# Performance work log

Hardware: AMD Instinct MI355X
Metric: run time of the kernel (lower is better)

Reference implementation:

```python
import jax, jax.numpy as jnp
import numpy as np

P, N, B, F, H, O, D, A = 3, 6144, 3072, 512, 8, 32, 256, 128
HI = F // H  # per-head input dim = 64


def setup_inputs() -> dict:
    key = jax.random.key(0)
    ks = jax.random.split(key, 12)
    s = 0.05
    return dict(
        features=jax.random.normal(ks[0], (P, N, F), jnp.float32),
        biases=jax.random.normal(ks[1], (P, N, N), jnp.float32),
        batch_nodes=jax.random.randint(ks[2], (P, B), 0, N),
        RL_thresholds=jax.random.uniform(ks[3], (P, 1), jnp.float32),
        Wc1=jax.random.normal(ks[4], (P, H, O, HI), jnp.float32) * s,
        bc1=jnp.zeros((P, H, O), jnp.float32),
        a1=jax.random.normal(ks[5], (P, H, O), jnp.float32) * s,
        ab1=jnp.zeros((P, H), jnp.float32),
        a2=jax.random.normal(ks[6], (P, H, O), jnp.float32) * s,
        ab2=jnp.zeros((P, H), jnp.float32),
        Wm=jax.random.normal(ks[7], (D, D), jnp.float32) * s,
        bm=jnp.zeros((D,), jnp.float32),
        w_omega=jax.random.normal(ks[8], (D, A), jnp.float32) * s,
        b_omega=jnp.zeros((A,), jnp.float32),
        u_omega=jax.random.normal(ks[9], (A,), jnp.float32) * s,
    )


def reference(features, biases, batch_nodes, RL_thresholds, Wc1, bc1, a1, ab1,
              a2, ab2, Wm, bm, w_omega, b_omega, u_omega):
    embeds = []
    for i in range(P):  # fixed small relation loop (bias_mx_len)
        idx = batch_nodes[i]
        bf = features[i][idx]                      # [B, F]
        bb = biases[i][idx][:, idx]                # [B, B] bias mask
        xh = bf.reshape(B, H, HI).transpose(1, 0, 2)   # [H, B, HI] per-head feature slices
        # Attn_Head: conv1d(k=1) == per-head linear projection
        seq = jnp.einsum('hbi,hoi->hbo', xh, Wc1[i]) + bc1[i][:, None, :]  # [H, B, O]
        f1 = jnp.einsum('hbo,ho->hb', seq, a1[i]) + ab1[i][:, None]       # [H, B]
        f2 = jnp.einsum('hbo,ho->hb', seq, a2[i]) + ab2[i][:, None]       # [H, B]
        logits = jax.nn.leaky_relu(f1[:, :, None] + f2[:, None, :], 0.01)  # [H, B, B]
        coefs = jax.nn.softmax(logits + bb[None], axis=-1)                 # [H, B, B]
        out = jax.nn.elu(jnp.einsum('hqk,hko->hqo', coefs, seq))           # [H, B, O]
        h1 = out.transpose(1, 0, 2).reshape(B, H * O)                      # concat heads -> [B, D]
        embeds.append(h1 @ Wm.T + bm)                                      # w_multi
    multi = jnp.stack(embeds, axis=1)              # [B, P, D]
    inputs = multi * RL_thresholds[None]           # RL scaling, [P,1] broadcasts
    # SimpleAttnLayer: semantic attention over relations
    v = jnp.tanh(jnp.einsum('bpd,da->bpa', inputs, w_omega) + b_omega)
    vu = jnp.einsum('bpa,a->bp', v, u_omega)
    alphas = jax.nn.softmax(vu, axis=-1)           # [B, P]
    return jnp.sum(inputs * alphas[:, :, None], axis=1)  # [B, D]
```

## Files before the change

### kernel.cpp

```cpp
#include <hip/hip_runtime.h>
#include <cstdint>
#include <cstddef>

#define PP 3
#define NN 6144
#define BB 3072
#define FF 512
#define HH 8
#define OO 32
#define DD 256
#define AA 128
#define M0 10.0f
#define KSPLIT 4
#define KRANGE (BB/KSPLIT)
#define NT (KRANGE/32)

typedef __attribute__((ext_vector_type(8))) short short8;
typedef __attribute__((ext_vector_type(4))) float f32x4;

__device__ __forceinline__ unsigned short f2bf(float x){
  union { float f; unsigned u; } v; v.f = x;
  unsigned r = v.u + 0x7fffu + ((v.u >> 16) & 1u);
  return (unsigned short)(r >> 16);
}

__device__ __forceinline__ f32x4 mfma16(short8 a, short8 b, f32x4 c){
  return __builtin_amdgcn_mfma_f32_16x16x32_bf16(a, b, c, 0, 0, 0);
}

__global__ __launch_bounds__(256) void k_seq(
    const float* __restrict__ features, const int* __restrict__ batch_nodes,
    const float* __restrict__ Wc1, const float* __restrict__ bc1,
    const float* __restrict__ a1, const float* __restrict__ ab1,
    const float* __restrict__ a2, const float* __restrict__ ab2,
    unsigned short* __restrict__ seqT, float* __restrict__ f1g, float* __restrict__ f2T)
{
  int i = blockIdx.z, h = blockIdx.y, b0 = blockIdx.x * 8;
  int t = threadIdx.x;
  __shared__ float xs[8][64];
  __shared__ float wt[64][33];
  __shared__ float a1s[32], a2s[32], bcs[32];
  __shared__ float sst[32][9];
  const float* W = Wc1 + (size_t)(i*HH + h) * OO * 64;
  for (int e = t; e < 2048; e += 256){ int o = e >> 6, c = e & 63; wt[c][o] = W[e]; }
  if (t < 32){
    a1s[t] = a1[(i*HH+h)*OO + t];
    a2s[t] = a2[(i*HH+h)*OO + t];
    bcs[t] = bc1[(i*HH+h)*OO + t];
  }
  for (int e = t; e < 512; e += 256){
    int bl = e >> 6, c = e & 63;
    int row = batch_nodes[i*BB + b0 + bl];
    xs[bl][c] = features[((size_t)i*NN + row)*FF + h*64 + c];
  }
  __syncthreads();
  int bl = t >> 5, o = t & 31;
  float acc = bcs[o];
  #pragma unroll
  for (int c = 0; c < 64; c++) acc += xs[bl][c] * wt[c][o];
  float v1 = acc * a1s[o], v2 = acc * a2s[o];
  #pragma unroll
  for (int s = 16; s >= 1; s >>= 1){ v1 += __shfl_xor(v1, s); v2 += __shfl_xor(v2, s); }
  if (o == 0){
    f1g[(i*HH+h)*BB + b0 + bl] = v1 + ab1[i*HH+h];
    f2T[((size_t)i*BB + b0 + bl)*HH + h] = v2 + ab2[i*HH+h];
  }
  sst[o][bl] = acc;
  __syncthreads();
  {
    int o2 = t >> 3, b2 = t & 7;
    seqT[((size_t)(i*HH+h)*OO + o2)*BB + b0 + b2] = f2bf(sst[o2][b2]);
  }
}

__global__ __launch_bounds__(256) void k_gather(
    const float* __restrict__ biases, const int* __restrict__ batch_nodes,
    const float* __restrict__ f1g, const float* __restrict__ f2T,
    float* __restrict__ bbg, float* __restrict__ linv, int i_base, int nbuf)
{
  int i = i_base + blockIdx.z;
  int q0 = blockIdx.x * 2;
  int t = threadIdx.x;
  __shared__ float rowbuf[2][NN];
  __shared__ float wred[4][2][HH];
  int r0 = batch_nodes[i*BB + q0];
  int r1 = batch_nodes[i*BB + q0 + 1];
  const float4* s0 = (const float4*)(biases + ((size_t)i*NN + r0)*NN);
  const float4* s1 = (const float4*)(biases + ((size_t)i*NN + r1)*NN);
  #pragma unroll
  for (int e = 0; e < NN/4; e += 256){
    ((float4*)rowbuf[0])[e + t] = s0[e + t];
    ((float4*)rowbuf[1])[e + t] = s1[e + t];
  }
  float f1h[2][HH], lh[2][HH];
  #pragma unroll
  for (int h = 0; h < HH; h++){
    f1h[0][h] = f1g[(i*HH+h)*BB + q0];
    f1h[1][h] = f1g[(i*HH+h)*BB + q0 + 1];
    lh[0][h] = 0.f; lh[1][h] = 0.f;
  }
  const int* ci = batch_nodes + i*BB;
  float* dst0 = bbg + ((size_t)(i % nbuf)*BB + q0)*BB;
  float* dst1 = dst0 + BB;
  __syncthreads();
  for (int c = 0; c < BB; c += 256){
    int k = c + t;
    int col = ci[k];
    float b0v = rowbuf[0][col];
    float b1v = rowbuf[1][col];
    dst0[k] = b0v; dst1[k] = b1v;
    const float4* fp = (const float4*)(f2T + ((size_t)i*BB + k)*HH);
    float4 fa = fp[0], fb = fp[1];
    float f2v[8] = {fa.x,fa.y,fa.z,fa.w,fb.x,fb.y,fb.z,fb.w};
    #pragma unroll
    for (int h = 0; h < HH; h++){
      float s0v = f1h[0][h] + f2v[h]; s0v = (s0v >= 0.f ? s0v : 0.01f*s0v) + b0v;
      float s1v = f1h[1][h] + f2v[h]; s1v = (s1v >= 0.f ? s1v : 0.01f*s1v) + b1v;
      lh[0][h] += __expf(s0v - M0);
      lh[1][h] += __expf(s1v - M0);
    }
  }
  #pragma unroll
  for (int r = 0; r < 2; r++)
  #pragma unroll
  for (int h = 0; h < HH; h++){
    float v = lh[r][h];
    #pragma unroll
    for (int s = 32; s >= 1; s >>= 1) v += __shfl_xor(v, s);
    if ((t & 63) == 0) wred[t >> 6][r][h] = v;
  }
  __syncthreads();
  if (t < 16){
    int r = t >> 3, h = t & 7;
    float L = wred[0][r][h] + wred[1][r][h] + wred[2][r][h] + wred[3][r][h];
    linv[(i*HH+h)*BB + q0 + r] = 1.f / L;
  }
}

__global__ __launch_bounds__(256, 4) void k_attn(
    const float* __restrict__ bbg, const unsigned short* __restrict__ seqT,
    const float* __restrict__ f1g, const float* __restrict__ f2T,
    const float* __restrict__ linv, float* __restrict__ h1p, int i_base, int nbuf)
{
  int i = i_base + blockIdx.z;
  int ks = blockIdx.y;
  int q0 = blockIdx.x * 32;
  int kbase = ks * KRANGE;
  int t = threadIdx.x;
  int w = t >> 6, lane = t & 63;
  int qf = lane & 15, kq = lane >> 4;
  __shared__ float bbt[2][32][33];
  __shared__ float f2t[2][32][9];
  f32x4 acc[2][2][2] = {};
  float f1r[2][2], lir[2][2];
  #pragma unroll
  for (int hh = 0; hh < 2; hh++)
  #pragma unroll
  for (int qh = 0; qh < 2; qh++){
    int h = w*2 + hh;
    f1r[hh][qh] = f1g[(i*HH+h)*BB + q0 + qh*16 + qf];
    lir[hh][qh] = linv[(i*HH+h)*BB + q0 + qh*16 + qf];
  }
  const float* bbb = bbg + (size_t)(i % nbuf)*BB*BB;

  auto ld = [&](int k0, float rb[4], float &rf, short8 rs[4]){
    #pragma unroll
    for (int j = 0; j < 4; j++){ int e = j*256 + t; int r = e >> 5, c = e & 31;
      rb[j] = bbb[(size_t)(q0 + r)*BB + k0 + c]; }
    { int c = t >> 3, h = t & 7; rf = f2T[((size_t)i*BB + k0 + c)*HH + h]; }
    #pragma unroll
    for (int hh = 0; hh < 2; hh++){
      const unsigned short* sp = seqT + ((size_t)(i*HH + w*2 + hh)*OO)*BB + k0 + kq*8;
      rs[hh*2+0] = *(const short8*)(sp + (size_t)qf*BB);
      rs[hh*2+1] = *(const short8*)(sp + (size_t)(qf+16)*BB);
    }
  };
  auto st = [&](int buf, float rb[4], float rf){
    #pragma unroll
    for (int j = 0; j < 4; j++){ int e = j*256 + t; int r = e >> 5, c = e & 31; bbt[buf][r][c] = rb[j]; }
    { int c = t >> 3, h = t & 7; f2t[buf][c][h] = rf; }
  };
  auto comp = [&](int buf, short8 rs[4]){
    #pragma unroll
    for (int hh = 0; hh < 2; hh++){
      int h = w*2 + hh;
      int kk = kq*8;
      short8 af0, af1;
      #pragma unroll
      for (int j = 0; j < 8; j++){
        float f2v = f2t[buf][kk+j][h];
        float s0 = f1r[hh][0] + f2v; s0 = (s0 >= 0.f ? s0 : 0.01f*s0) + bbt[buf][qf][kk+j];
        float s1 = f1r[hh][1] + f2v; s1 = (s1 >= 0.f ? s1 : 0.01f*s1) + bbt[buf][qf+16][kk+j];
        af0[j] = (short)f2bf(__expf(s0 - M0) * lir[hh][0]);
        af1[j] = (short)f2bf(__expf(s1 - M0) * lir[hh][1]);
      }
      acc[hh][0][0] = mfma16(af0, rs[hh*2+0], acc[hh][0][0]);
      acc[hh][0][1] = mfma16(af0, rs[hh*2+1], acc[hh][0][1]);
      acc[hh][1][0] = mfma16(af1, rs[hh*2+0], acc[hh][1][0]);
      acc[hh][1][1] = mfma16(af1, rs[hh*2+1], acc[hh][1][1]);
    }
  };

  float rbbA[4], rf2A; short8 rsqA[4];
  float rbbB[4], rf2B; short8 rsqB[4];
  ld(kbase, rbbA, rf2A, rsqA);
  st(0, rbbA, rf2A);
  __syncthreads();
  for (int it = 0; it < NT; it += 2){
    int k1 = kbase + (it+1)*32;
    int k2 = (it+2 < NT) ? kbase + (it+2)*32 : kbase;
    ld(k1, rbbB, rf2B, rsqB);
    comp(0, rsqA);
    st(1, rbbB, rf2B);
    __syncthreads();
    ld(k2, rbbA, rf2A, rsqA);
    comp(1, rsqB);
    st(0, rbbA, rf2A);
    __syncthreads();
  }
  #pragma unroll
  for (int hh = 0; hh < 2; hh++){
    int h = w*2 + hh;
    #pragma unroll
    for (int qh = 0; qh < 2; qh++)
    #pragma unroll
    for (int oh = 0; oh < 2; oh++)
    #pragma unroll
    for (int r = 0; r < 4; r++){
      int q = q0 + qh*16 + kq*4 + r;
      int o = qf + oh*16;
      h1p[(((size_t)ks*PP + i)*BB + q)*DD + h*OO + o] = acc[hh][qh][oh][r];
    }
  }
}

__global__ __launch_bounds__(256) void k_twm(const float* __restrict__ Wm, float* __restrict__ wmT){
  int e = blockIdx.x, d = threadIdx.x;
  wmT[(size_t)e*DD + d] = Wm[(size_t)d*DD + e];
}

__global__ __launch_bounds__(256) void k_final(
    const float* __restrict__ h1p, const float* __restrict__ wmT, const float* __restrict__ bm,
    const float* __restrict__ RL, const float* __restrict__ w_omega, const float* __restrict__ b_omega,
    const float* __restrict__ u_omega, float* __restrict__ out)
{
  __shared__ float buf[48*256];
  __shared__ float wred[4][24];
  __shared__ float alph[3][16];
  const size_t PB = (size_t)PP*BB*DD;
  int t = threadIdx.x;
  int lane = t & 63, w = t >> 6;
  int b0 = blockIdx.x * 16;
  for (int e = t; e < 48*256; e += 256){
    int pb = e >> 8, d = e & 255;
    int p = pb / 16, bl = pb & 15;
    size_t off = ((size_t)p*BB + b0 + bl)*DD + d;
    float v = h1p[off] + h1p[off + PB] + h1p[off + 2*PB] + h1p[off + 3*PB];
    buf[e] = (v > 0.f) ? v : (__expf(v) - 1.f);
  }
  __syncthreads();
  float acc[48];
  #pragma unroll
  for (int x = 0; x < 48; x++) acc[x] = 0.f;
  for (int e = 0; e < 256; e += 4){
    float w0 = wmT[(e+0)*DD + t];
    float w1 = wmT[(e+1)*DD + t];
    float w2 = wmT[(e+2)*DD + t];
    float w3 = wmT[(e+3)*DD + t];
    #pragma unroll
    for (int pb = 0; pb < 48; pb++){
      float4 hv = *(const float4*)&buf[pb*256 + e];
      acc[pb] += hv.x*w0 + hv.y*w1 + hv.z*w2 + hv.w*w3;
    }
  }
  __syncthreads();
  {
    float bmv = bm[t];
    #pragma unroll
    for (int p = 0; p < 3; p++){
      float rl = RL[p];
      #pragma unroll
      for (int bl = 0; bl < 16; bl++)
        buf[(p*16+bl)*256 + t] = (acc[p*16+bl] + bmv) * rl;
    }
  }
  __syncthreads();
  int a = t & 127, g = t >> 7;
  float acc2[24];
  #pragma unroll
  for (int x = 0; x < 24; x++) acc2[x] = 0.f;
  for (int e = 0; e < 256; e += 4){
    float w0 = w_omega[(e+0)*AA + a];
    float w1 = w_omega[(e+1)*AA + a];
    float w2 = w_omega[(e+2)*AA + a];
    float w3 = w_omega[(e+3)*AA + a];
    #pragma unroll
    for (int p = 0; p < 3; p++){
      #pragma unroll
      for (int bl = 0; bl < 8; bl++){
        float4 iv = *(const float4*)&buf[(p*16 + g*8 + bl)*256 + e];
        acc2[p*8+bl] += iv.x*w0 + iv.y*w1 + iv.z*w2 + iv.w*w3;
      }
    }
  }
  {
    float bo = b_omega[a], uo = u_omega[a];
    #pragma unroll
    for (int x = 0; x < 24; x++){
      float v = tanhf(acc2[x] + bo) * uo;
      #pragma unroll
      for (int s = 32; s >= 1; s >>= 1) v += __shfl_xor(v, s);
      if (lane == 0) wred[w][x] = v;
    }
  }
  __syncthreads();
  if (t < 16){
    int b = t;
    int g2 = b >> 3, bl2 = b & 7;
    float vu[3];
    #pragma unroll
    for (int p = 0; p < 3; p++){
      int j = p*8 + bl2;
      vu[p] = wred[g2*2 + 0][j] + wred[g2*2 + 1][j];
    }
    float mx = fmaxf(vu[0], fmaxf(vu[1], vu[2]));
    float e0 = __expf(vu[0]-mx), e1 = __expf(vu[1]-mx), e2 = __expf(vu[2]-mx);
    float inv = 1.f / (e0+e1+e2);
    alph[0][b] = e0*inv; alph[1][b] = e1*inv; alph[2][b] = e2*inv;
  }
  __syncthreads();
  #pragma unroll
  for (int bl = 0; bl < 16; bl++){
    float o = buf[(0*16+bl)*256 + t]*alph[0][bl]
            + buf[(1*16+bl)*256 + t]*alph[1][bl]
            + buf[(2*16+bl)*256 + t]*alph[2][bl];
    out[(size_t)(b0+bl)*DD + t] = o;
  }
}

extern "C" void kernel_launch(void* const* d_in, const int* in_sizes, int n_in,
                              void* d_out, int out_size, void* d_ws, size_t ws_size,
                              hipStream_t stream)
{
  const float* features = (const float*)d_in[0];
  const float* biases   = (const float*)d_in[1];
  const int*   batch_nodes = (const int*)d_in[2];
  const float* RL   = (const float*)d_in[3];
  const float* Wc1  = (const float*)d_in[4];
  const float* bc1  = (const float*)d_in[5];
  const float* a1   = (const float*)d_in[6];
  const float* ab1  = (const float*)d_in[7];
  const float* a2   = (const float*)d_in[8];
  const float* ab2  = (const float*)d_in[9];
  const float* Wm   = (const float*)d_in[10];
  const float* bm   = (const float*)d_in[11];
  const float* w_omega = (const float*)d_in[12];
  const float* b_omega = (const float*)d_in[13];
  const float* u_omega = (const float*)d_in[14];
  float* out = (float*)d_out;

  size_t sz_bbg1 = (size_t)BB*BB*4;
  size_t sz_seqT = (size_t)PP*HH*OO*BB*2;
  size_t sz_f    = (size_t)PP*HH*BB*4;
  size_t sz_h1   = (size_t)PP*BB*DD*4;
  size_t sz_wmT  = (size_t)DD*DD*4;
  size_t fixed = sz_seqT + 3*sz_f + (size_t)KSPLIT*sz_h1 + sz_wmT + 16*256;
  int nbuf = (ws_size >= fixed + 3*sz_bbg1 + 256) ? 3 : 1;

  char* p = (char*)d_ws;
  auto take = [&](size_t bytes)->char*{ char* r = p; p += (bytes + 255) & ~(size_t)255; return r; };
  float* bbg  = (float*)take(sz_bbg1 * (size_t)nbuf);
  unsigned short* seqT = (unsigned short*)take(sz_seqT);
  float* f1g  = (float*)take(sz_f);
  float* f2T  = (float*)take(sz_f);
  float* linv = (float*)take(sz_f);
  float* h1p  = (float*)take(sz_h1 * (size_t)KSPLIT);
  float* wmT  = (float*)take(sz_wmT);

  k_twm<<<dim3(DD), dim3(DD), 0, stream>>>(Wm, wmT);
  k_seq<<<dim3(BB/8, HH, PP), dim3(256), 0, stream>>>(features, batch_nodes, Wc1, bc1, a1, ab1, a2, ab2, seqT, f1g, f2T);
  int nloop = (nbuf == 3) ? 1 : 3;
  int z = (nbuf == 3) ? 3 : 1;
  for (int r = 0; r < nloop; r++){
    k_gather<<<dim3(BB/2, 1, z), dim3(256), 0, stream>>>(biases, batch_nodes, f1g, f2T, bbg, linv, r, nbuf);
    k_attn<<<dim3(BB/32, KSPLIT, z), dim3(256), 0, stream>>>(bbg, seqT, f1g, f2T, linv, h1p, r, nbuf);
  }
  k_final<<<dim3(BB/16), dim3(256), 0, stream>>>(h1p, wmT, bm, RL, w_omega, b_omega, u_omega, out);
}
```

Before: 928.1 us.

## Defer softmax normalization: accumulate row sums in attention kernel, normalize in final

Removes the per-row exp-sum pass from the gather kernel, which now only copies and pre-shifts the bias by M0. The attention kernel accumulates unnormalized exp sums alongside the MFMA products, writes per-split partial sums, and the final kernel divides the combined output by the summed denominators before ELU. This cuts a full pass of exp work over B×B×H elements and the f2T reads in gather. The cost is extra adds in the attention inner loop and a small extra buffer. Precision changes slightly because unnormalized values are rounded to bf16 before the MFMA, and the bf16 conversion now uses the library intrinsic instead of the hand-written rounding.

After: 1.093 ms. +17.8%, slower.

```diff
diff --git a/kernel.cpp b/kernel.cpp
--- a/kernel.cpp
+++ b/kernel.cpp
@@ -1,4 +1,5 @@
 #include <hip/hip_runtime.h>
+#include <hip/hip_bf16.h>
 #include <cstdint>
 #include <cstddef>
 
@@ -24,6 +25,10 @@
   return (unsigned short)(r >> 16);
 }
 
+__device__ __forceinline__ short f2bf_n(float x){
+  return __builtin_bit_cast(short, __float2bfloat16(x));
+}
+
 __device__ __forceinline__ f32x4 mfma16(short8 a, short8 b, f32x4 c){
   return __builtin_amdgcn_mfma_f32_16x16x32_bf16(a, b, c, 0, 0, 0);
 }
@@ -75,14 +80,12 @@
 
 __global__ __launch_bounds__(256) void k_gather(
     const float* __restrict__ biases, const int* __restrict__ batch_nodes,
-    const float* __restrict__ f1g, const float* __restrict__ f2T,
-    float* __restrict__ bbg, float* __restrict__ linv, int i_base, int nbuf)
+    float* __restrict__ bbg, int i_base, int nbuf)
 {
   int i = i_base + blockIdx.z;
   int q0 = blockIdx.x * 2;
   int t = threadIdx.x;
   __shared__ float rowbuf[2][NN];
-  __shared__ float wred[4][2][HH];
   int r0 = batch_nodes[i*BB + q0];
   int r1 = batch_nodes[i*BB + q0 + 1];
   const float4* s0 = (const float4*)(biases + ((size_t)i*NN + r0)*NN);
@@ -92,55 +95,23 @@
     ((float4*)rowbuf[0])[e + t] = s0[e + t];
     ((float4*)rowbuf[1])[e + t] = s1[e + t];
   }
-  float f1h[2][HH], lh[2][HH];
-  #pragma unroll
-  for (int h = 0; h < HH; h++){
-    f1h[0][h] = f1g[(i*HH+h)*BB + q0];
-    f1h[1][h] = f1g[(i*HH+h)*BB + q0 + 1];
-    lh[0][h] = 0.f; lh[1][h] = 0.f;
-  }
   const int* ci = batch_nodes + i*BB;
   float* dst0 = bbg + ((size_t)(i % nbuf)*BB + q0)*BB;
   float* dst1 = dst0 + BB;
   __syncthreads();
+  #pragma unroll 4
   for (int c = 0; c < BB; c += 256){
     int k = c + t;
     int col = ci[k];
-    float b0v = rowbuf[0][col];
-    float b1v = rowbuf[1][col];
-    dst0[k] = b0v; dst1[k] = b1v;
-    const float4* fp = (const float4*)(f2T + ((size_t)i*BB + k)*HH);
-    float4 fa = fp[0], fb = fp[1];
-    float f2v[8] = {fa.x,fa.y,fa.z,fa.w,fb.x,fb.y,fb.z,fb.w};
-    #pragma unroll
-    for (int h = 0; h < HH; h++){
-      float s0v = f1h[0][h] + f2v[h]; s0v = (s0v >= 0.f ? s0v : 0.01f*s0v) + b0v;
-      float s1v = f1h[1][h] + f2v[h]; s1v = (s1v >= 0.f ? s1v : 0.01f*s1v) + b1v;
-      lh[0][h] += __expf(s0v - M0);
-      lh[1][h] += __expf(s1v - M0);
-    }
-  }
-  #pragma unroll
-  for (int r = 0; r < 2; r++)
-  #pragma unroll
-  for (int h = 0; h < HH; h++){
-    float v = lh[r][h];
-    #pragma unroll
-    for (int s = 32; s >= 1; s >>= 1) v += __shfl_xor(v, s);
-    if ((t & 63) == 0) wred[t >> 6][r][h] = v;
-  }
-  __syncthreads();
-  if (t < 16){
-    int r = t >> 3, h = t & 7;
-    float L = wred[0][r][h] + wred[1][r][h] + wred[2][r][h] + wred[3][r][h];
-    linv[(i*HH+h)*BB + q0 + r] = 1.f / L;
+    dst0[k] = rowbuf[0][col] - M0;
+    dst1[k] = rowbuf[1][col] - M0;
   }
 }
 
 __global__ __launch_bounds__(256, 4) void k_attn(
     const float* __restrict__ bbg, const unsigned short* __restrict__ seqT,
     const float* __restrict__ f1g, const float* __restrict__ f2T,
-    const float* __restrict__ linv, float* __restrict__ h1p, int i_base, int nbuf)
+    float* __restrict__ Lp, float* __restrict__ h1p, int i_base, int nbuf)
 {
   int i = i_base + blockIdx.z;
   int ks = blockIdx.y;
@@ -152,14 +123,14 @@
   __shared__ float bbt[2][32][33];
   __shared__ float f2t[2][32][9];
   f32x4 acc[2][2][2] = {};
-  float f1r[2][2], lir[2][2];
+  float Ls[2][2] = {{0.f,0.f},{0.f,0.f}};
+  float f1r[2][2];
   #pragma unroll
   for (int hh = 0; hh < 2; hh++)
   #pragma unroll
   for (int qh = 0; qh < 2; qh++){
     int h = w*2 + hh;
     f1r[hh][qh] = f1g[(i*HH+h)*BB + q0 + qh*16 + qf];
-    lir[hh][qh] = linv[(i*HH+h)*BB + q0 + qh*16 + qf];
   }
   const float* bbb = bbg + (size_t)(i % nbuf)*BB*BB;
 
@@ -191,8 +162,10 @@
         float f2v = f2t[buf][kk+j][h];
         float s0 = f1r[hh][0] + f2v; s0 = (s0 >= 0.f ? s0 : 0.01f*s0) + bbt[buf][qf][kk+j];
         float s1 = f1r[hh][1] + f2v; s1 = (s1 >= 0.f ? s1 : 0.01f*s1) + bbt[buf][qf+16][kk+j];
-        af0[j] = (short)f2bf(__expf(s0 - M0) * lir[hh][0]);
-        af1[j] = (short)f2bf(__expf(s1 - M0) * lir[hh][1]);
+        float e0 = __expf(s0), e1 = __expf(s1);
+        Ls[hh][0] += e0; Ls[hh][1] += e1;
+        af0[j] = f2bf_n(e0);
+        af1[j] = f2bf_n(e1);
       }
       acc[hh][0][0] = mfma16(af0, rs[hh*2+0], acc[hh][0][0]);
       acc[hh][0][1] = mfma16(af0, rs[hh*2+1], acc[hh][0][1]);
@@ -219,6 +192,16 @@
     __syncthreads();
   }
   #pragma unroll
+  for (int hh = 0; hh < 2; hh++)
+  #pragma unroll
+  for (int qh = 0; qh < 2; qh++){
+    float v = Ls[hh][qh];
+    v += __shfl_xor(v, 16);
+    v += __shfl_xor(v, 32);
+    if (kq == 0)
+      Lp[(((size_t)ks*PP + i)*HH + w*2 + hh)*BB + q0 + qh*16 + qf] = v;
+  }
+  #pragma unroll
   for (int hh = 0; hh < 2; hh++){
     int h = w*2 + hh;
     #pragma unroll
@@ -240,22 +223,34 @@
 }
 
 __global__ __launch_bounds__(256) void k_final(
-    const float* __restrict__ h1p, const float* __restrict__ wmT, const float* __restrict__ bm,
+    const float* __restrict__ h1p, const float* __restrict__ Lp,
+    const float* __restrict__ wmT, const float* __restrict__ bm,
     const float* __restrict__ RL, const float* __restrict__ w_omega, const float* __restrict__ b_omega,
     const float* __restrict__ u_omega, float* __restrict__ out)
 {
   __shared__ float buf[48*256];
   __shared__ float wred[4][24];
   __shared__ float alph[3][16];
+  __shared__ float linvs[48][8];
   const size_t PB = (size_t)PP*BB*DD;
+  const size_t KL = (size_t)PP*HH*BB;
   int t = threadIdx.x;
   int lane = t & 63, w = t >> 6;
   int b0 = blockIdx.x * 16;
+  for (int e = t; e < 48*8; e += 256){
+    int pb = e >> 3, h = e & 7;
+    int p = pb / 16, bl = pb & 15;
+    size_t off = ((size_t)p*HH + h)*BB + b0 + bl;
+    float L = Lp[off] + Lp[off+KL] + Lp[off+2*KL] + Lp[off+3*KL];
+    linvs[pb][h] = 1.f / L;
+  }
+  __syncthreads();
   for (int e = t; e < 48*256; e += 256){
     int pb = e >> 8, d = e & 255;
     int p = pb / 16, bl = pb & 15;
     size_t off = ((size_t)p*BB + b0 + bl)*DD + d;
     float v = h1p[off] + h1p[off + PB] + h1p[off + 2*PB] + h1p[off + 3*PB];
+    v *= linvs[pb][d >> 5];
     buf[e] = (v > 0.f) ? v : (__expf(v) - 1.f);
   }
   __syncthreads();
@@ -364,7 +359,8 @@
   size_t sz_f    = (size_t)PP*HH*BB*4;
   size_t sz_h1   = (size_t)PP*BB*DD*4;
   size_t sz_wmT  = (size_t)DD*DD*4;
-  size_t fixed = sz_seqT + 3*sz_f + (size_t)KSPLIT*sz_h1 + sz_wmT + 16*256;
+  size_t sz_Lp   = (size_t)KSPLIT*PP*HH*BB*4;
+  size_t fixed = sz_seqT + 2*sz_f + (size_t)KSPLIT*sz_h1 + sz_wmT + sz_Lp + 16*256;
   int nbuf = (ws_size >= fixed + 3*sz_bbg1 + 256) ? 3 : 1;
 
   char* p = (char*)d_ws;
@@ -373,7 +369,7 @@
   unsigned short* seqT = (unsigned short*)take(sz_seqT);
   float* f1g  = (float*)take(sz_f);
   float* f2T  = (float*)take(sz_f);
-  float* linv = (float*)take(sz_f);
+  float* Lp   = (float*)take(sz_Lp);
   float* h1p  = (float*)take(sz_h1 * (size_t)KSPLIT);
   float* wmT  = (float*)take(sz_wmT);
 
@@ -382,8 +378,8 @@
   int nloop = (nbuf == 3) ? 1 : 3;
   int z = (nbuf == 3) ? 3 : 1;
   for (int r = 0; r < nloop; r++){
-    k_gather<<<dim3(BB/2, 1, z), dim3(256), 0, stream>>>(biases, batch_nodes, f1g, f2T, bbg, linv, r, nbuf);
-    k_attn<<<dim3(BB/32, KSPLIT, z), dim3(256), 0, stream>>>(bbg, seqT, f1g, f2T, linv, h1p, r, nbuf);
-  }
-  k_final<<<dim3(BB/16), dim3(256), 0, stream>>>(h1p, wmT, bm, RL, w_omega, b_omega, u_omega, out);
-}
+    k_gather<<<dim3(BB/2, 1, z), dim3(256), 0, stream>>>(biases, batch_nodes, bbg, r, nbuf);
+    k_attn<<<dim3(BB/32, KSPLIT, z), dim3(256), 0, stream>>>(bbg, seqT, f1g, f2T, Lp, h1p, r, nbuf);
+  }
+  k_final<<<dim3(BB/16), dim3(256), 0, stream>>>(h1p, Lp, wmT, bm, RL, w_omega, b_omega, u_omega, out);
+}
```
